# Kernel tuning notes

Measured on AMD Instinct MI355X. Metric: run time of the kernel, lower is better.

## Reference

```python
import jax, jax.numpy as jnp
import numpy as np

N = 200000      # active voxels
K = 27          # kernel volume (3x3x3)
M = 50000       # rulebook pairs per kernel offset
CIN = 64
COUT = 64


def setup_inputs() -> dict:
    key = jax.random.key(0)
    k1, k2, k3, k4 = jax.random.split(key, 4)
    feats = jax.random.normal(k1, (N, CIN), dtype=jnp.float32)
    std = 1.0 / np.sqrt(CIN * K)
    kernel = jax.random.uniform(k2, (K, CIN, COUT), dtype=jnp.float32,
                                minval=-std, maxval=std)
    in_map = jax.random.randint(k3, (K, M), 0, N, dtype=jnp.int32)
    out_map = jax.random.randint(k4, (K, M), 0, N, dtype=jnp.int32)
    return {"feats": feats, "kernel": kernel, "in_map": in_map, "out_map": out_map}


def reference(feats, kernel, in_map, out_map):
    # gather: [K, M, Cin]
    gathered = feats[in_map]
    # per-offset GEMM: [K, M, Cout]
    partial = jnp.einsum('kmi,kio->kmo', gathered, kernel)
    # scatter-add into output features [N, Cout]
    out = jnp.zeros((feats.shape[0], kernel.shape[-1]), dtype=feats.dtype)
    out = out.at[out_map].add(partial)
    return out
```

## Files before the change

### kernel.cpp

```cpp
#include <hip/hip_runtime.h>
#include <hip/hip_fp16.h>

#define CIN   64
#define COUT  64

typedef __attribute__((ext_vector_type(8))) short bf16x8;
typedef __attribute__((ext_vector_type(4))) float f32x4;
typedef __attribute__((ext_vector_type(4))) unsigned u32x4;

__device__ inline unsigned short f2bf(float f) {
    unsigned u = __float_as_uint(f);
    return (unsigned short)((u + 0x7FFFu + ((u >> 16) & 1u)) >> 16);
}

__device__ inline unsigned pack_h2(float lo, float hi) {
    __half l = __float2half(lo), h = __float2half(hi);
    return (unsigned)__half_as_ushort(l) | ((unsigned)__half_as_ushort(h) << 16);
}

__device__ inline float2 h2f2(unsigned v) {
    return make_float2(
        __half2float(__ushort_as_half((unsigned short)(v & 0xFFFFu))),
        __half2float(__ushort_as_half((unsigned short)(v >> 16))));
}

__global__ __launch_bounds__(256)
void cvt_hist(const f32x4* __restrict__ in, unsigned short* __restrict__ outb,
              int n8, const int* __restrict__ out_map, int total,
              int* __restrict__ cnt, int* __restrict__ rk) {
    int i = blockIdx.x * 256 + threadIdx.x;
    if (i < n8) {
        f32x4 f0 = __builtin_nontemporal_load(&in[2 * i]);
        f32x4 f1 = __builtin_nontemporal_load(&in[2 * i + 1]);
        bf16x8 o;
        o[0] = (short)f2bf(f0[0]); o[1] = (short)f2bf(f0[1]);
        o[2] = (short)f2bf(f0[2]); o[3] = (short)f2bf(f0[3]);
        o[4] = (short)f2bf(f1[0]); o[5] = (short)f2bf(f1[1]);
        o[6] = (short)f2bf(f1[2]); o[7] = (short)f2bf(f1[3]);
        *(bf16x8*)(outb + 8 * (size_t)i) = o;
    }
    if (i < total)
        rk[i] = atomicAdd(&cnt[out_map[i]], 1);
}

__global__ __launch_bounds__(256)
void scanA(const int* __restrict__ cnt, int* __restrict__ excl,
           int* __restrict__ blocksum, int N) {
    __shared__ int sm[256];
    const int b = blockIdx.x, t = threadIdx.x;
    const int base = b * 1024 + t * 4;
    int v0 = (base + 0 < N) ? cnt[base + 0] : 0;
    int v1 = (base + 1 < N) ? cnt[base + 1] : 0;
    int v2 = (base + 2 < N) ? cnt[base + 2] : 0;
    int v3 = (base + 3 < N) ? cnt[base + 3] : 0;
    const int s = v0 + v1 + v2 + v3;
    sm[t] = s; __syncthreads();
    for (int off = 1; off < 256; off <<= 1) {
        int x = (t >= off) ? sm[t - off] : 0;
        __syncthreads();
        sm[t] += x;
        __syncthreads();
    }
    const int e = sm[t] - s;
    if (t == 255) blocksum[b] = sm[t];
    if (base + 0 < N) excl[base + 0] = e;
    if (base + 1 < N) excl[base + 1] = e + v0;
    if (base + 2 < N) excl[base + 2] = e + v0 + v1;
    if (base + 3 < N) excl[base + 3] = e + v0 + v1 + v2;
}

__global__ __launch_bounds__(256)
void scanB(const int* __restrict__ blocksum, int* __restrict__ blockbase,
           int nb, int* __restrict__ total_out) {
    __shared__ int sm[256];
    const int t = threadIdx.x;
    const int s = (t < nb) ? blocksum[t] : 0;
    sm[t] = s; __syncthreads();
    for (int off = 1; off < 256; off <<= 1) {
        int x = (t >= off) ? sm[t - off] : 0;
        __syncthreads();
        sm[t] += x;
        __syncthreads();
    }
    if (t < nb) blockbase[t] = sm[t] - s;
    if (t == 255) *total_out = sm[255];
}

__global__ __launch_bounds__(256)
void scanC(int* __restrict__ offsets, const int* __restrict__ blockbase, int N,
           int nblk, const float* __restrict__ weight,
           unsigned short* __restrict__ wb, int kvol) {
    const int b = blockIdx.x;
    if (b < nblk) {
        int i = b * 256 + threadIdx.x;
        if (i < N) offsets[i] += blockbase[i >> 10];
        return;
    }
    const int idx = (b - nblk) * 256 + threadIdx.x;
    if (idx >= kvol * 64 * 8) return;
    const int k   = idx >> 9;
    const int rem = idx & 511;
    const int n   = rem >> 3;
    const int c0  = (rem & 7) << 3;
    const float* __restrict__ wk = weight + (size_t)k * (CIN * COUT);
    unsigned short* __restrict__ dst = wb + ((size_t)k * 64 + n) * 64 + c0;
#pragma unroll
    for (int j = 0; j < 8; ++j)
        dst[j] = f2bf(wk[(c0 + j) * COUT + n]);
}

__global__ __launch_bounds__(256, 8)
void spconv_phase1(const unsigned short* __restrict__ featsb,
                   const unsigned short* __restrict__ wb,
                   const int*            __restrict__ in_map,
                   const int*            __restrict__ out_map,
                   const int*            __restrict__ offsets,
                   const int*            __restrict__ rk,
                   unsigned*             __restrict__ partial_dw,
                   int M) {
    const int k      = blockIdx.y;
    const int tid    = threadIdx.x;
    const int lane   = tid & 63;
    const int m      = lane & 15;
    const int quad   = lane >> 4;
    const int wave   = blockIdx.x * 4 + (tid >> 6);
    const int nwaves = gridDim.x * 4;

    const unsigned short* __restrict__ wkb = wb + (size_t)k * (CIN * COUT);
    bf16x8 afrag[4][2];
#pragma unroll
    for (int t = 0; t < 4; ++t) {
        const int n = 16 * (m >> 2) + 4 * t + (m & 3);
#pragma unroll
        for (int h = 0; h < 2; ++h)
            afrag[t][h] = *(const bf16x8*)(wkb + n * 64 + 32 * h + 8 * quad);
    }

    const int base   = k * M;
    const int ntiles = M >> 4;

    int t0 = wave, t1 = wave + nwaves, t2 = wave + 2 * nwaves;

    int ir0 = 0, orow0 = 0, rk0 = 0;
    if (t0 < ntiles) {
        const int p = base + (t0 << 4) + m;
        ir0 = in_map[p]; orow0 = out_map[p]; rk0 = rk[p];
    }
    int slt0 = 0; bf16x8 a0_0 = {}, a1_0 = {};
    if (t0 < ntiles) {
        if (quad == 0) slt0 = offsets[orow0] + rk0;
        const unsigned short* fb = featsb + ((size_t)ir0 << 6) + 8 * quad;
        a0_0 = *(const bf16x8*)fb;
        a1_0 = *(const bf16x8*)(fb + 32);
    }
    int ir1 = 0, orow1 = 0, rk1 = 0;
    if (t1 < ntiles) {
        const int p = base + (t1 << 4) + m;
        ir1 = in_map[p]; orow1 = out_map[p]; rk1 = rk[p];
    }

    while (t0 < ntiles) {
        int slt1 = 0; bf16x8 a0_1 = {}, a1_1 = {};
        if (t1 < ntiles) {
            if (quad == 0) slt1 = offsets[orow1] + rk1;
            const unsigned short* fb = featsb + ((size_t)ir1 << 6) + 8 * quad;
            a0_1 = *(const bf16x8*)fb;
            a1_1 = *(const bf16x8*)(fb + 32);
        }
        int ir2 = 0, orow2 = 0, rk2 = 0;
        if (t2 < ntiles) {
            const int p = base + (t2 << 4) + m;
            ir2 = in_map[p]; orow2 = out_map[p]; rk2 = rk[p];
        }

        f32x4 acc[4];
#pragma unroll
        for (int t = 0; t < 4; ++t) {
            acc[t] = {0.f, 0.f, 0.f, 0.f};
            acc[t] = __builtin_amdgcn_mfma_f32_16x16x32_bf16(afrag[t][0], a0_0, acc[t], 0, 0, 0);
            acc[t] = __builtin_amdgcn_mfma_f32_16x16x32_bf16(afrag[t][1], a1_0, acc[t], 0, 0, 0);
        }

        const int s = __shfl(slt0, m);
        unsigned d[8];
#pragma unroll
        for (int t = 0; t < 4; ++t) {
            d[2 * t]     = pack_h2(acc[t][0], acc[t][1]);
            d[2 * t + 1] = pack_h2(acc[t][2], acc[t][3]);
        }
        uint4* dst = (uint4*)(partial_dw + (size_t)s * 32 + 8 * quad);
        dst[0] = make_uint4(d[0], d[1], d[2], d[3]);
        dst[1] = make_uint4(d[4], d[5], d[6], d[7]);

        t0 = t1; t1 = t2; t2 += nwaves;
        slt0 = slt1; a0_0 = a0_1; a1_0 = a1_1;
        ir1 = ir2; orow1 = orow2; rk1 = rk2;
    }
}

__global__ __launch_bounds__(256)
void spconv_phase2(const u32x4* __restrict__ partial_q,
                   const int*   __restrict__ offsets,
                   float4*      __restrict__ out4,
                   int nrows) {
    const int tid  = threadIdx.x;
    const int lane = tid & 63;
    const int g    = lane >> 3;
    const int q    = lane & 7;
    const int wave = blockIdx.x * 4 + (tid >> 6);
    const int nw   = gridDim.x * 4;

    if (wave >= nrows) return;
    int cur_s = offsets[wave];
    int cur_e = offsets[wave + 1];

    for (int r = wave; r < nrows; r += nw) {
        const int start = cur_s;
        const int c     = cur_e - start;
        const int rn    = r + nw;
        if (rn < nrows) {
            cur_s = offsets[rn];
            cur_e = offsets[rn + 1];
        }

        float s0 = 0.f, s1 = 0.f, s2 = 0.f, s3 = 0.f;
        float s4 = 0.f, s5 = 0.f, s6 = 0.f, s7 = 0.f;
        for (int j0 = 0; j0 < c; j0 += 8) {
            const int j = j0 + g;
            if (j < c) {
                const u32x4 v = __builtin_nontemporal_load(
                    &partial_q[(size_t)(start + j) * 8 + q]);
                const float2 f0 = h2f2(v[0]), f1 = h2f2(v[1]);
                const float2 f2 = h2f2(v[2]), f3 = h2f2(v[3]);
                s0 += f0.x; s1 += f0.y; s2 += f1.x; s3 += f1.y;
                s4 += f2.x; s5 += f2.y; s6 += f3.x; s7 += f3.y;
            }
        }

#pragma unroll
        for (int msk = 8; msk <= 32; msk <<= 1) {
            s0 += __shfl_xor(s0, msk); s1 += __shfl_xor(s1, msk);
            s2 += __shfl_xor(s2, msk); s3 += __shfl_xor(s3, msk);
            s4 += __shfl_xor(s4, msk); s5 += __shfl_xor(s5, msk);
            s6 += __shfl_xor(s6, msk); s7 += __shfl_xor(s7, msk);
        }

        if (g == 0) {
            out4[(size_t)r * 16 + 2 * q]     = make_float4(s0, s1, s2, s3);
            out4[(size_t)r * 16 + 2 * q + 1] = make_float4(s4, s5, s6, s7);
        }
    }
}

__global__ __launch_bounds__(256)
void spconv_atomic(const float* __restrict__ feats,
                   const float* __restrict__ weight,
                   const int*   __restrict__ in_map,
                   const int*   __restrict__ out_map,
                   float*       __restrict__ out,
                   int M) {
    const int k      = blockIdx.y;
    const int tid    = threadIdx.x;
    const int lane   = tid & 63;
    const int m      = lane & 15;
    const int quad   = lane >> 4;
    const int wave   = blockIdx.x * 4 + (tid >> 6);
    const int nwaves = gridDim.x * 4;

    const float* __restrict__ wk = weight + (size_t)k * (CIN * COUT);
    bf16x8 bfrag[4][2];
#pragma unroll
    for (int t = 0; t < 4; ++t)
#pragma unroll
        for (int h = 0; h < 2; ++h) {
            const int n  = 16 * t + m;
            const int c0 = 32 * h + 8 * quad;
#pragma unroll
            for (int j = 0; j < 8; ++j)
                bfrag[t][h][j] = (short)f2bf(wk[(c0 + j) * COUT + n]);
        }

    const int base   = k * M;
    const int ntiles = M >> 4;

    for (int tile = wave; tile < ntiles; tile += nwaves) {
        const int p0 = tile << 4;
        const int in_row  = in_map[base + p0 + m];
        const int out_row = out_map[base + p0 + m];

        const float* __restrict__ fr = feats + ((size_t)in_row << 6) + 8 * quad;
        const f32x4 f0 = *(const f32x4*)(fr + 0);
        const f32x4 f1 = *(const f32x4*)(fr + 4);
        const f32x4 f2 = *(const f32x4*)(fr + 32);
        const f32x4 f3 = *(const f32x4*)(fr + 36);

        bf16x8 a0, a1;
#pragma unroll
        for (int j = 0; j < 4; ++j) {
            a0[j]     = (short)f2bf(f0[j]);
            a0[j + 4] = (short)f2bf(f1[j]);
            a1[j]     = (short)f2bf(f2[j]);
            a1[j + 4] = (short)f2bf(f3[j]);
        }

        int orow[4];
#pragma unroll
        for (int r = 0; r < 4; ++r)
            orow[r] = __shfl(out_row, 4 * quad + r);

        f32x4 acc[4];
#pragma unroll
        for (int t = 0; t < 4; ++t) {
            acc[t] = {0.f, 0.f, 0.f, 0.f};
            acc[t] = __builtin_amdgcn_mfma_f32_16x16x32_bf16(a0, bfrag[t][0], acc[t], 0, 0, 0);
            acc[t] = __builtin_amdgcn_mfma_f32_16x16x32_bf16(a1, bfrag[t][1], acc[t], 0, 0, 0);
        }

#pragma unroll
        for (int t = 0; t < 4; ++t)
#pragma unroll
            for (int r = 0; r < 4; ++r)
                atomicAdd(out + (size_t)orow[r] * COUT + 16 * t + m, acc[t][r]);
    }
}

__global__ __launch_bounds__(256)
void zero_out_kernel(float4* __restrict__ out, int n4) {
    int i = blockIdx.x * 256 + threadIdx.x;
    if (i < n4) out[i] = make_float4(0.f, 0.f, 0.f, 0.f);
}

static inline size_t al256(size_t x) { return (x + 255) & ~(size_t)255; }

extern "C" void kernel_launch(void* const* d_in, const int* in_sizes, int n_in,
                              void* d_out, int out_size, void* d_ws, size_t ws_size,
                              hipStream_t stream) {
    const float* feats   = (const float*)d_in[0];
    const float* weight  = (const float*)d_in[1];
    const int*   in_map  = (const int*)d_in[2];
    const int*   out_map = (const int*)d_in[3];
    float*       out     = (float*)d_out;

    const int K     = in_sizes[1] / (CIN * COUT);
    const int M     = in_sizes[2] / K;
    const int N     = out_size / COUT;
    const int total = K * M;
    const int nb    = (N + 1023) >> 10;

    const size_t off_b  = al256((size_t)(N + 1) * 4);
    const size_t cnt_b  = al256((size_t)N * 4);
    const size_t bs_b   = al256((size_t)nb * 4);
    const size_t bb_b   = al256((size_t)nb * 4);
    const size_t rank_b = al256((size_t)total * 4);
    const size_t wb_b   = al256((size_t)K * CIN * COUT * 2);
    const size_t fb_b   = al256((size_t)N * CIN * 2);
    const size_t part_b = (size_t)total * COUT * 2;
    const size_t need   = off_b + cnt_b + bs_b + bb_b + rank_b + wb_b + fb_b + part_b;

    if ((M & 15) == 0 && nb <= 256 && ws_size >= need) {
        char* p = (char*)d_ws;
        int*            offsets   = (int*)p;            p += off_b;
        int*            cnt       = (int*)p;            p += cnt_b;
        int*            blocksum  = (int*)p;            p += bs_b;
        int*            blockbase = (int*)p;            p += bb_b;
        int*            rk        = (int*)p;            p += rank_b;
        unsigned short* wb        = (unsigned short*)p; p += wb_b;
        unsigned short* featsb    = (unsigned short*)p; p += fb_b;
        unsigned*       partial   = (unsigned*)p;

        const int n8 = N * CIN / 8;
        const int fused_n = (n8 > total) ? n8 : total;

        (void)hipMemsetAsync(cnt, 0, (size_t)N * 4, stream);
        cvt_hist<<<(fused_n + 255) / 256, 256, 0, stream>>>(
            (const f32x4*)feats, featsb, n8, out_map, total, cnt, rk);
        scanA<<<nb, 256, 0, stream>>>(cnt, offsets, blocksum, N);
        scanB<<<1, 256, 0, stream>>>(blocksum, blockbase, nb, offsets + N);

        const int nblkC = (N + 255) / 256;
        const int nwblk = (K * 64 * 8 + 255) / 256;
        scanC<<<nblkC + nwblk, 256, 0, stream>>>(offsets, blockbase, N,
                                                 nblkC, weight, wb, K);

        dim3 g1(160, K);
        spconv_phase1<<<g1, 256, 0, stream>>>(featsb, wb, in_map, out_map,
                                              offsets, rk, partial, M);

        spconv_phase2<<<8192, 256, 0, stream>>>((const u32x4*)partial, offsets,
                                                (float4*)out, N);
        return;
    }

    int n4 = out_size / 4;
    zero_out_kernel<<<(n4 + 255) / 256, 256, 0, stream>>>((float4*)out, n4);
    dim3 grid(80, K);
    spconv_atomic<<<grid, 256, 0, stream>>>(feats, weight, in_map, out_map, out, M);
}
```

Measured before the change: 304.0 us.

## Write GEMM partials in pair order and gather via index list in reduction

Phase 1 now writes each pair's fp16 partial row at its natural pair index, where before it scattered each row to a sorted slot. A new fill_idx kernel builds a slot-to-pair index array from the histogram offsets and ranks. Phase 2 then gathers partials indirectly through that array. This trades scattered 128-byte writes in phase 1 for scattered reads in phase 2, and adds one extra small kernel and an index read per row. The phase-1 grid is halved, its occupancy hint is dropped, and the nontemporal load hint in phase 2 is removed.

Result: no change. 306.8 us (+0.9%).

```diff
diff --git a/kernel.cpp b/kernel.cpp
--- a/kernel.cpp
+++ b/kernel.cpp
@@ -109,13 +109,19 @@
         dst[j] = f2bf(wk[(c0 + j) * COUT + n]);
 }
 
-__global__ __launch_bounds__(256, 8)
+__global__ __launch_bounds__(256)
+void fill_idx(const int* __restrict__ out_map, const int* __restrict__ rk,
+              const int* __restrict__ offsets, int* __restrict__ idx,
+              int total) {
+    int p = blockIdx.x * 256 + threadIdx.x;
+    if (p < total)
+        idx[offsets[out_map[p]] + rk[p]] = p;
+}
+
+__global__ __launch_bounds__(256)
 void spconv_phase1(const unsigned short* __restrict__ featsb,
                    const unsigned short* __restrict__ wb,
                    const int*            __restrict__ in_map,
-                   const int*            __restrict__ out_map,
-                   const int*            __restrict__ offsets,
-                   const int*            __restrict__ rk,
                    unsigned*             __restrict__ partial_dw,
                    int M) {
     const int k      = blockIdx.y;
@@ -141,37 +147,26 @@
 
     int t0 = wave, t1 = wave + nwaves, t2 = wave + 2 * nwaves;
 
-    int ir0 = 0, orow0 = 0, rk0 = 0;
+    int ir0 = 0;
+    if (t0 < ntiles) ir0 = in_map[base + (t0 << 4) + m];
+    bf16x8 a0_0 = {}, a1_0 = {};
     if (t0 < ntiles) {
-        const int p = base + (t0 << 4) + m;
-        ir0 = in_map[p]; orow0 = out_map[p]; rk0 = rk[p];
-    }
-    int slt0 = 0; bf16x8 a0_0 = {}, a1_0 = {};
-    if (t0 < ntiles) {
-        if (quad == 0) slt0 = offsets[orow0] + rk0;
         const unsigned short* fb = featsb + ((size_t)ir0 << 6) + 8 * quad;
         a0_0 = *(const bf16x8*)fb;
         a1_0 = *(const bf16x8*)(fb + 32);
     }
-    int ir1 = 0, orow1 = 0, rk1 = 0;
-    if (t1 < ntiles) {
-        const int p = base + (t1 << 4) + m;
-        ir1 = in_map[p]; orow1 = out_map[p]; rk1 = rk[p];
-    }
+    int ir1 = 0;
+    if (t1 < ntiles) ir1 = in_map[base + (t1 << 4) + m];
 
     while (t0 < ntiles) {
-        int slt1 = 0; bf16x8 a0_1 = {}, a1_1 = {};
+        bf16x8 a0_1 = {}, a1_1 = {};
         if (t1 < ntiles) {
-            if (quad == 0) slt1 = offsets[orow1] + rk1;
             const unsigned short* fb = featsb + ((size_t)ir1 << 6) + 8 * quad;
             a0_1 = *(const bf16x8*)fb;
             a1_1 = *(const bf16x8*)(fb + 32);
         }
-        int ir2 = 0, orow2 = 0, rk2 = 0;
-        if (t2 < ntiles) {
-            const int p = base + (t2 << 4) + m;
-            ir2 = in_map[p]; orow2 = out_map[p]; rk2 = rk[p];
-        }
+        int ir2 = 0;
+        if (t2 < ntiles) ir2 = in_map[base + (t2 << 4) + m];
 
         f32x4 acc[4];
 #pragma unroll
@@ -181,25 +176,26 @@
             acc[t] = __builtin_amdgcn_mfma_f32_16x16x32_bf16(afrag[t][1], a1_0, acc[t], 0, 0, 0);
         }
 
-        const int s = __shfl(slt0, m);
+        const size_t pair = (size_t)base + ((size_t)t0 << 4) + m;
         unsigned d[8];
 #pragma unroll
         for (int t = 0; t < 4; ++t) {
             d[2 * t]     = pack_h2(acc[t][0], acc[t][1]);
             d[2 * t + 1] = pack_h2(acc[t][2], acc[t][3]);
         }
-        uint4* dst = (uint4*)(partial_dw + (size_t)s * 32 + 8 * quad);
+        uint4* dst = (uint4*)(partial_dw + pair * 32 + 8 * quad);
         dst[0] = make_uint4(d[0], d[1], d[2], d[3]);
         dst[1] = make_uint4(d[4], d[5], d[6], d[7]);
 
         t0 = t1; t1 = t2; t2 += nwaves;
-        slt0 = slt1; a0_0 = a0_1; a1_0 = a1_1;
-        ir1 = ir2; orow1 = orow2; rk1 = rk2;
+        a0_0 = a0_1; a1_0 = a1_1;
+        ir1 = ir2;
     }
 }
 
 __global__ __launch_bounds__(256)
 void spconv_phase2(const u32x4* __restrict__ partial_q,
+                   const int*   __restrict__ idx,
                    const int*   __restrict__ offsets,
                    float4*      __restrict__ out4,
                    int nrows) {
@@ -228,8 +224,8 @@
         for (int j0 = 0; j0 < c; j0 += 8) {
             const int j = j0 + g;
             if (j < c) {
-                const u32x4 v = __builtin_nontemporal_load(
-                    &partial_q[(size_t)(start + j) * 8 + q]);
+                const int pj = idx[start + j];
+                const u32x4 v = partial_q[(size_t)pj * 8 + q];
                 const float2 f0 = h2f2(v[0]), f1 = h2f2(v[1]);
                 const float2 f2 = h2f2(v[2]), f3 = h2f2(v[3]);
                 s0 += f0.x; s1 += f0.y; s2 += f1.x; s3 += f1.y;
@@ -352,10 +348,12 @@
     const size_t bs_b   = al256((size_t)nb * 4);
     const size_t bb_b   = al256((size_t)nb * 4);
     const size_t rank_b = al256((size_t)total * 4);
+    const size_t idx_b  = al256((size_t)total * 4);
     const size_t wb_b   = al256((size_t)K * CIN * COUT * 2);
     const size_t fb_b   = al256((size_t)N * CIN * 2);
     const size_t part_b = (size_t)total * COUT * 2;
-    const size_t need   = off_b + cnt_b + bs_b + bb_b + rank_b + wb_b + fb_b + part_b;
+    const size_t need   = off_b + cnt_b + bs_b + bb_b + rank_b + idx_b
+                        + wb_b + fb_b + part_b;
 
     if ((M & 15) == 0 && nb <= 256 && ws_size >= need) {
         char* p = (char*)d_ws;
@@ -364,6 +362,7 @@
         int*            blocksum  = (int*)p;            p += bs_b;
         int*            blockbase = (int*)p;            p += bb_b;
         int*            rk        = (int*)p;            p += rank_b;
+        int*            idx       = (int*)p;            p += idx_b;
         unsigned short* wb        = (unsigned short*)p; p += wb_b;
         unsigned short* featsb    = (unsigned short*)p; p += fb_b;
         unsigned*       partial   = (unsigned*)p;
@@ -381,13 +380,14 @@
         const int nwblk = (K * 64 * 8 + 255) / 256;
         scanC<<<nblkC + nwblk, 256, 0, stream>>>(offsets, blockbase, N,
                                                  nblkC, weight, wb, K);
-
-        dim3 g1(160, K);
-        spconv_phase1<<<g1, 256, 0, stream>>>(featsb, wb, in_map, out_map,
-                                              offsets, rk, partial, M);
-
-        spconv_phase2<<<8192, 256, 0, stream>>>((const u32x4*)partial, offsets,
-                                                (float4*)out, N);
+        fill_idx<<<(total + 255) / 256, 256, 0, stream>>>(out_map, rk, offsets,
+                                                          idx, total);
+
+        dim3 g1(80, K);
+        spconv_phase1<<<g1, 256, 0, stream>>>(featsb, wb, in_map, partial, M);
+
+        spconv_phase2<<<8192, 256, 0, stream>>>((const u32x4*)partial, idx,
+                                                offsets, (float4*)out, N);
         return;
     }
 
```
